# Kernel optimization log

Hardware: AMD Instinct MI355X
Metric: run time of the kernel (lower is better)

Reference implementation:

```python
import math
import jax, jax.numpy as jnp
import numpy as np

N = 50000          # nodes
E = 1_600_000      # edges
DNE = 128
DED = 128
NUM_RBF = 50
R_CUT = 5.0
LN_EPS = 1e-5


def setup_inputs() -> dict:
    key = jax.random.key(0)
    ks = jax.random.split(key, 16)
    z = jax.random.normal(ks[0], (N, 25), jnp.float32)
    edge = jax.random.randint(ks[1], (E, 2), 0, N, dtype=jnp.int64)
    r = jax.random.uniform(ks[2], (E,), jnp.float32) * (R_CUT * 1.1)  # some beyond cutoff
    u_raw = jax.random.normal(ks[3], (E, 3), jnp.float32)
    u = u_raw / jnp.linalg.norm(u_raw, axis=-1, keepdims=True)

    def xavier(k, shape):
        fan_in, fan_out = shape
        lim = math.sqrt(6.0 / (fan_in + fan_out))
        return jax.random.uniform(k, shape, jnp.float32, -lim, lim)

    return {
        "z": z, "edge": edge, "r": r, "u": u,
        "A_na_w": xavier(ks[4], (25, DNE)), "A_na_b": jnp.zeros((DNE,), jnp.float32),
        "A_nbr_w": xavier(ks[5], (25, DNE)), "A_nbr_b": jnp.zeros((DNE,), jnp.float32),
        "W_ndp_w": xavier(ks[6], (NUM_RBF, DNE)), "W_ndp_b": jnp.zeros((DNE,), jnp.float32),
        "W_nrd_w": xavier(ks[7], (2 * DNE, DNE)), "W_nrd_b": jnp.zeros((DNE,), jnp.float32),
        "W_nru_w": xavier(ks[8], (DNE, DNE)), "W_nru_b": jnp.zeros((DNE,), jnp.float32),
        "W_erp_w": xavier(ks[9], (NUM_RBF, DED)), "W_erp_b": jnp.zeros((DED,), jnp.float32),
        "ln_g": jnp.ones((DNE,), jnp.float32), "ln_b": jnp.zeros((DNE,), jnp.float32),
    }


def _sh_l2(u):
    x, y, zc = u[:, 0], u[:, 1], u[:, 2]
    s3 = math.sqrt(3.0)
    return jnp.stack([
        s3 * x * y,
        s3 * y * zc,
        0.5 * (3.0 * zc * zc - 1.0),
        s3 * zc * x,
        0.5 * s3 * (x * x - y * y),
    ], axis=-1)  # [E, 5]


def _rbf(r):
    start = math.exp(-R_CUT)
    means = jnp.linspace(start, 1.0, NUM_RBF)
    beta = (2.0 / NUM_RBF * (1.0 - start)) ** (-2)
    alpha = 5.0 / R_CUT
    return jnp.exp(-beta * (jnp.exp(-alpha * r[:, None]) - means) ** 2)  # [E, NUM_RBF]


def reference(z, edge, r, u,
              A_na_w, A_na_b, A_nbr_w, A_nbr_b,
              W_ndp_w, W_ndp_b, W_nrd_w, W_nrd_b,
              W_nru_w, W_nru_b, W_erp_w, W_erp_b,
              ln_g, ln_b):
    i, j = edge[:, 0], edge[:, 1]
    n_nodes = z.shape[0]

    # edge tensor representations (Lmax=2)
    rt0 = r[:, None]          # [E,1]
    rt1 = u                   # [E,3]
    rt2 = _sh_l2(u)           # [E,5]

    rbf = _rbf(r)                                              # [E,R]
    c = (0.5 * (jnp.cos(math.pi * r / R_CUT) + 1.0)
         * (r < R_CUT).astype(r.dtype))[:, None]               # [E,1]

    nbr = jax.nn.silu(z @ A_nbr_w + A_nbr_b)                   # [N,dne]
    gate = (rbf @ W_ndp_w + W_ndp_b) * c                       # [E,dne]
    msg = nbr[j] * gate                                        # gather + gate
    m = jax.ops.segment_sum(msg, i, num_segments=n_nodes)      # scatter-add [N,dne]

    na = jax.nn.silu(z @ A_na_w + A_na_b)
    h = jnp.concatenate([na, m], axis=-1) @ W_nrd_w + W_nrd_b  # [N,dne]
    mu = jnp.mean(h, axis=-1, keepdims=True)
    var = jnp.var(h, axis=-1, keepdims=True)
    h = (h - mu) / jnp.sqrt(var + LN_EPS) * ln_g + ln_b
    h = jax.nn.silu(h)
    h = h @ W_nru_w + W_nru_b                                  # [N,dne]

    t = (h[i] + h[j]) * (rbf @ W_erp_w + W_erp_b)              # [E,ded]
    return (h, t, rt0, rt1, rt2, c)
```

## Files before the change

### kernel.cpp

```cpp
#include <hip/hip_runtime.h>
#include <hip/hip_bf16.h>
#include <math.h>

#define NN 50000
#define NE 1600000
#define D 128
#define NRBF 50
#define RCUT 5.0f
#define LNEPS 1e-5f
#define SCAN_B 196
#define NB 16
#define NPW 8
#define EO_GRID 2048

typedef __attribute__((ext_vector_type(8))) short bf16x8;
typedef __attribute__((ext_vector_type(4))) float f32x4;

__device__ __forceinline__ float silu_f(float x) {
    return x / (1.0f + __expf(-x));
}
__device__ __forceinline__ unsigned short f2bf(float x) {
    __hip_bfloat16 b = __float2bfloat16(x);
    return *reinterpret_cast<unsigned short*>(&b);
}
__device__ __forceinline__ float bf2f(unsigned short u) {
    unsigned int x = ((unsigned int)u) << 16;
    return __uint_as_float(x);
}

__global__ __launch_bounds__(128) void nbr_kernel(
    const float* __restrict__ z, const float* __restrict__ Aw,
    const float* __restrict__ Ab, unsigned short* __restrict__ nbr_bf)
{
    const int n = blockIdx.x;
    const int d = threadIdx.x;
    float acc = Ab[d];
#pragma unroll
    for (int k = 0; k < 25; ++k)
        acc = fmaf(z[n * 25 + k], Aw[k * D + d], acc);
    nbr_bf[(size_t)n * D + d] = f2bf(silu_f(acc));
}

__global__ __launch_bounds__(256) void aux_kernel(
    const int* __restrict__ edge, const float* __restrict__ r,
    const float* __restrict__ u, float* __restrict__ rt0,
    float* __restrict__ rt1, float* __restrict__ rt2,
    float* __restrict__ cout, int* __restrict__ cnt)
{
    const int e = blockIdx.x * 256 + threadIdx.x;
    if (e >= NE) return;
    const float rr = r[e];
    __builtin_nontemporal_store(rr, &rt0[e]);
    const float cc = (rr < RCUT)
        ? 0.5f * (__cosf(3.14159265358979f * rr * (1.0f / RCUT)) + 1.0f)
        : 0.0f;
    __builtin_nontemporal_store(cc, &cout[e]);
    const float x  = u[e * 3 + 0];
    const float y  = u[e * 3 + 1];
    const float zc = u[e * 3 + 2];
    __builtin_nontemporal_store(x,  &rt1[(size_t)e * 3 + 0]);
    __builtin_nontemporal_store(y,  &rt1[(size_t)e * 3 + 1]);
    __builtin_nontemporal_store(zc, &rt1[(size_t)e * 3 + 2]);
    const float s3 = 1.7320508075688772f;
    __builtin_nontemporal_store(s3 * x * y,                  &rt2[(size_t)e * 5 + 0]);
    __builtin_nontemporal_store(s3 * y * zc,                 &rt2[(size_t)e * 5 + 1]);
    __builtin_nontemporal_store(0.5f * (3.0f * zc * zc - 1.0f), &rt2[(size_t)e * 5 + 2]);
    __builtin_nontemporal_store(s3 * zc * x,                 &rt2[(size_t)e * 5 + 3]);
    __builtin_nontemporal_store(0.5f * s3 * (x * x - y * y), &rt2[(size_t)e * 5 + 4]);
    atomicAdd(&cnt[edge[2 * e]], 1);
}

__global__ __launch_bounds__(256) void scan1_kernel(
    const int* __restrict__ cnt, int* __restrict__ off, int* __restrict__ bsum)
{
    __shared__ int s[2][256];
    const int t = threadIdx.x;
    const int g = blockIdx.x * 256 + t;
    const int v = (g < NN) ? cnt[g] : 0;
    int incl = v;
    s[0][t] = incl;
    __syncthreads();
    int cur = 0;
#pragma unroll
    for (int dd = 1; dd < 256; dd <<= 1) {
        const int add = (t >= dd) ? s[cur][t - dd] : 0;
        incl += add;
        s[cur ^ 1][t] = incl;
        __syncthreads();
        cur ^= 1;
    }
    if (g < NN) off[g] = incl - v;
    if (t == 255) bsum[blockIdx.x] = incl;
}

__global__ __launch_bounds__(256) void scan2_kernel(int* __restrict__ bsum)
{
    __shared__ int s[2][256];
    const int t = threadIdx.x;
    const int v = (t < SCAN_B) ? bsum[t] : 0;
    int incl = v;
    s[0][t] = incl;
    __syncthreads();
    int cur = 0;
#pragma unroll
    for (int dd = 1; dd < 256; dd <<= 1) {
        const int add = (t >= dd) ? s[cur][t - dd] : 0;
        incl += add;
        s[cur ^ 1][t] = incl;
        __syncthreads();
        cur ^= 1;
    }
    if (t < SCAN_B) bsum[t] = incl - v;
}

__global__ __launch_bounds__(256) void scan3_kernel(
    int* __restrict__ off, const int* __restrict__ bsum)
{
    const int g = blockIdx.x * 256 + threadIdx.x;
    if (g < NN) off[g] += bsum[blockIdx.x];
    if (g == 0) off[NN] = NE;
}

__global__ __launch_bounds__(256) void scatter_kernel(
    const int* __restrict__ edge, const float* __restrict__ r,
    const int* __restrict__ off, int* __restrict__ cursor,
    uint2* __restrict__ jr)
{
    const int e = blockIdx.x * 256 + threadIdx.x;
    if (e >= NE) return;
    const int2 ep = ((const int2*)edge)[e];
    const int pos = atomicAdd(&cursor[ep.x], 1);
    uint2 v;
    v.x = (unsigned int)ep.y;
    v.y = __float_as_uint(r[e]);
    jr[off[ep.x] + pos] = v;
}

__global__ __launch_bounds__(256) void gather_msg_wave(
    const uint2* __restrict__ jr, const int* __restrict__ off,
    const float* __restrict__ W_ndp, const float* __restrict__ b_ndp,
    const unsigned short* __restrict__ nbr_bf, float* __restrict__ m)
{
    const int tid = threadIdx.x;
    const int w   = tid >> 6;
    const int l   = tid & 63;
    const int lr  = l & 15;
    const int lg  = l >> 4;

    bf16x8 wf[8][2];
#pragma unroll
    for (int dt = 0; dt < 8; ++dt) {
        const int col = lr * 8 + dt;
#pragma unroll
        for (int s = 0; s < 2; ++s) {
            bf16x8 v;
#pragma unroll
            for (int j = 0; j < 8; ++j) {
                const int k = s * 32 + lg * 8 + j;
                float wv = 0.0f;
                if (k < NRBF)       wv = W_ndp[k * D + col];
                else if (k == NRBF) wv = b_ndp[col];
                v[j] = (short)f2bf(wv);
            }
            wf[dt][s] = v;
        }
    }

    const float start = expf(-RCUT);
    const float step  = (1.0f - start) / (NRBF - 1);
    const float bq    = (2.0f / NRBF) * (1.0f - start);
    const float beta  = 1.0f / (bq * bq);

    const int wid = blockIdx.x * 4 + w;

    for (int nn = 0; nn < NPW; ++nn) {
        const int n = wid * NPW + nn;
        if (n >= NN) break;
        const int s0  = off[n];
        const int deg = off[n + 1] - s0;

        f32x4 macc[8] = {{0,0,0,0},{0,0,0,0},{0,0,0,0},{0,0,0,0},
                         {0,0,0,0},{0,0,0,0},{0,0,0,0},{0,0,0,0}};

        for (int base = 0; base < deg; base += 16) {
            unsigned int jv = 0;
            float er = 0.0f, cc = 0.0f;
            if (l < 16 && l < deg - base) {
                const uint2 v = jr[s0 + base + l];
                jv = v.x;
                const float rr = __uint_as_float(v.y);
                er = __expf(-rr);
                cc = (rr < RCUT)
                    ? 0.5f * (__cosf(3.14159265358979f * rr * (1.0f / RCUT)) + 1.0f)
                    : 0.0f;
            }
            const float erL = __shfl(er, lr);
            const float ccL = __shfl(cc, lr);

            bf16x8 af[2];
#pragma unroll
            for (int s = 0; s < 2; ++s) {
                bf16x8 a;
#pragma unroll
                for (int j = 0; j < 8; ++j) {
                    const int k = s * 32 + lg * 8 + j;
                    float pv = 0.0f;
                    if (k < NRBF) {
                        const float diff = erL - (start + (float)k * step);
                        pv = ccL * __expf(-beta * diff * diff);
                    } else if (k == NRBF) {
                        pv = ccL;
                    }
                    a[j] = (short)f2bf(pv);
                }
                af[s] = a;
            }

            f32x4 accs[8];
#pragma unroll
            for (int dt = 0; dt < 8; ++dt) {
                f32x4 acc = {0.0f, 0.0f, 0.0f, 0.0f};
                acc = __builtin_amdgcn_mfma_f32_16x16x32_bf16(af[0], wf[dt][0], acc, 0, 0, 0);
                acc = __builtin_amdgcn_mfma_f32_16x16x32_bf16(af[1], wf[dt][1], acc, 0, 0, 0);
                accs[dt] = acc;
            }
#pragma unroll
            for (int q = 0; q < 4; ++q) {
                const int jrow = __shfl((int)jv, lg * 4 + q);
                const bf16x8 nv8 = *(const bf16x8*)(nbr_bf + (size_t)jrow * D + lr * 8);
#pragma unroll
                for (int dt = 0; dt < 8; ++dt)
                    macc[dt][q] = fmaf(bf2f((unsigned short)nv8[dt]), accs[dt][q], macc[dt][q]);
            }
        }

        float vv[8];
#pragma unroll
        for (int dt = 0; dt < 8; ++dt) {
            float v = macc[dt][0] + macc[dt][1] + macc[dt][2] + macc[dt][3];
            v += __shfl_xor(v, 16);
            v += __shfl_xor(v, 32);
            vv[dt] = v;
        }
        if (lg == 0) {
            f32x4 o0 = {vv[0], vv[1], vv[2], vv[3]};
            f32x4 o1 = {vv[4], vv[5], vv[6], vv[7]};
            float* mp = &m[(size_t)n * D + lr * 8];
            *(f32x4*)mp       = o0;
            *(f32x4*)(mp + 4) = o1;
        }
    }
}

__global__ __launch_bounds__(256) void node_kernel2(
    const float* __restrict__ z, const float* __restrict__ A_na_w,
    const float* __restrict__ A_na_b, const float* __restrict__ m,
    const float* __restrict__ W_nrd_w, const float* __restrict__ W_nrd_b,
    const float* __restrict__ W_nru_w, const float* __restrict__ W_nru_b,
    const float* __restrict__ ln_g, const float* __restrict__ ln_b,
    float* __restrict__ hout, unsigned short* __restrict__ h_bf)
{
    __shared__ float inbuf[NB][260];
    __shared__ float wbuf[32][128];
    __shared__ float part[4][NB][2];

    const int tid = threadIdx.x;
    const int n0 = blockIdx.x * NB;
    const int nl = tid & 15;
    const int dg = tid >> 4;

    for (int idx = tid; idx < NB * 128; idx += 256) {
        const int n = idx >> 7;
        const int d = idx & 127;
        float acc = A_na_b[d];
#pragma unroll
        for (int k = 0; k < 25; ++k)
            acc = fmaf(z[(size_t)(n0 + n) * 25 + k], A_na_w[k * D + d], acc);
        inbuf[n][d]       = silu_f(acc);
        inbuf[n][128 + d] = m[(size_t)(n0 + n) * D + d];
    }

    float h1[8];
#pragma unroll
    for (int dd = 0; dd < 8; ++dd) h1[dd] = W_nrd_b[dg * 8 + dd];

    for (int tile = 0; tile < 8; ++tile) {
        __syncthreads();
        for (int v = tid; v < 32 * 32; v += 256) {
            const int row = v >> 5;
            const int c4  = (v & 31) * 4;
            *(float4*)&wbuf[row][c4] =
                *(const float4*)&W_nrd_w[(size_t)(tile * 32 + row) * D + c4];
        }
        __syncthreads();
#pragma unroll 4
        for (int k = 0; k < 32; ++k) {
            const float rin = inbuf[nl][tile * 32 + k];
            const float4 wa = *(const float4*)&wbuf[k][dg * 8];
            const float4 wb = *(const float4*)&wbuf[k][dg * 8 + 4];
            h1[0] = fmaf(rin, wa.x, h1[0]);
            h1[1] = fmaf(rin, wa.y, h1[1]);
            h1[2] = fmaf(rin, wa.z, h1[2]);
            h1[3] = fmaf(rin, wa.w, h1[3]);
            h1[4] = fmaf(rin, wb.x, h1[4]);
            h1[5] = fmaf(rin, wb.y, h1[5]);
            h1[6] = fmaf(rin, wb.z, h1[6]);
            h1[7] = fmaf(rin, wb.w, h1[7]);
        }
    }

    float s = 0.0f, sq = 0.0f;
#pragma unroll
    for (int dd = 0; dd < 8; ++dd) { s += h1[dd]; sq += h1[dd] * h1[dd]; }
    s  += __shfl_xor(s, 16);  sq += __shfl_xor(sq, 16);
    s  += __shfl_xor(s, 32);  sq += __shfl_xor(sq, 32);
    const int wv = tid >> 6;
    if ((tid & 63) < 16) { part[wv][nl][0] = s; part[wv][nl][1] = sq; }
    __syncthreads();
    float ts = 0.0f, tsq = 0.0f;
#pragma unroll
    for (int w = 0; w < 4; ++w) { ts += part[w][nl][0]; tsq += part[w][nl][1]; }
    const float mu  = ts * (1.0f / 128.0f);
    const float var = tsq * (1.0f / 128.0f) - mu * mu;
    const float inv = rsqrtf(var + LNEPS);

#pragma unroll
    for (int dd = 0; dd < 8; ++dd) {
        const int d = dg * 8 + dd;
        inbuf[nl][d] = silu_f((h1[dd] - mu) * inv * ln_g[d] + ln_b[d]);
    }

    float h2[8];
#pragma unroll
    for (int dd = 0; dd < 8; ++dd) h2[dd] = W_nru_b[dg * 8 + dd];

    for (int tile = 0; tile < 4; ++tile) {
        __syncthreads();
        for (int v = tid; v < 32 * 32; v += 256) {
            const int row = v >> 5;
            const int c4  = (v & 31) * 4;
            *(float4*)&wbuf[row][c4] =
                *(const float4*)&W_nru_w[(size_t)(tile * 32 + row) * D + c4];
        }
        __syncthreads();
#pragma unroll 4
        for (int k = 0; k < 32; ++k) {
            const float rin = inbuf[nl][tile * 32 + k];
            const float4 wa = *(const float4*)&wbuf[k][dg * 8];
            const float4 wb = *(const float4*)&wbuf[k][dg * 8 + 4];
            h2[0] = fmaf(rin, wa.x, h2[0]);
            h2[1] = fmaf(rin, wa.y, h2[1]);
            h2[2] = fmaf(rin, wa.z, h2[2]);
            h2[3] = fmaf(rin, wa.w, h2[3]);
            h2[4] = fmaf(rin, wb.x, h2[4]);
            h2[5] = fmaf(rin, wb.y, h2[5]);
            h2[6] = fmaf(rin, wb.z, h2[6]);
            h2[7] = fmaf(rin, wb.w, h2[7]);
        }
    }

    f32x4 o0 = {h2[0], h2[1], h2[2], h2[3]};
    f32x4 o1 = {h2[4], h2[5], h2[6], h2[7]};
    float* hp = &hout[(size_t)(n0 + nl) * D + dg * 8];
    __builtin_nontemporal_store(o0, (f32x4*)hp);
    __builtin_nontemporal_store(o1, (f32x4*)(hp + 4));

    unsigned int b0 = (unsigned int)f2bf(h2[0]) | ((unsigned int)f2bf(h2[1]) << 16);
    unsigned int b1 = (unsigned int)f2bf(h2[2]) | ((unsigned int)f2bf(h2[3]) << 16);
    unsigned int b2 = (unsigned int)f2bf(h2[4]) | ((unsigned int)f2bf(h2[5]) << 16);
    unsigned int b3 = (unsigned int)f2bf(h2[6]) | ((unsigned int)f2bf(h2[7]) << 16);
    *(uint4*)&h_bf[(size_t)(n0 + nl) * D + dg * 8] = make_uint4(b0, b1, b2, b3);
}

__global__ __launch_bounds__(256) void edge_out_wave(
    const int* __restrict__ edge, const float* __restrict__ r,
    const float* __restrict__ W_erp, const float* __restrict__ b_erp,
    const unsigned short* __restrict__ h_bf, float* __restrict__ t)
{
    const int tid = threadIdx.x;
    const int w   = tid >> 6;
    const int l   = tid & 63;
    const int lr  = l & 15;
    const int lg  = l >> 4;

    bf16x8 wf[8][2];
    float bias[8];
#pragma unroll
    for (int dt = 0; dt < 8; ++dt) {
        const int col = lr * 8 + dt;
        bias[dt] = b_erp[col];
#pragma unroll
        for (int s = 0; s < 2; ++s) {
            bf16x8 v;
#pragma unroll
            for (int j = 0; j < 8; ++j) {
                const int k = s * 32 + lg * 8 + j;
                v[j] = (k < NRBF) ? (short)f2bf(W_erp[k * D + col]) : (short)0;
            }
            wf[dt][s] = v;
        }
    }

    const float start = expf(-RCUT);
    const float step  = (1.0f - start) / (NRBF - 1);
    const float bq    = (2.0f / NRBF) * (1.0f - start);
    const float beta  = 1.0f / (bq * bq);

    const int wid = blockIdx.x * 4 + w;
    const int nw  = gridDim.x * 4;
    const int ngroup = NE / 16;

    for (int g = wid; g < ngroup; g += nw) {
        const int eb = g * 16;
        int iv = 0, jv = 0;
        float er = 0.0f;
        if (l < 16) {
            const int2 ep = ((const int2*)edge)[eb + l];
            iv = ep.x;
            jv = ep.y;
            er = __expf(-r[eb + l]);
        }
        const float erL = __shfl(er, lr);

        bf16x8 af[2];
#pragma unroll
        for (int s = 0; s < 2; ++s) {
            bf16x8 a;
#pragma unroll
            for (int j = 0; j < 8; ++j) {
                const int k = s * 32 + lg * 8 + j;
                float pv = 0.0f;
                if (k < NRBF) {
                    const float diff = erL - (start + (float)k * step);
                    pv = __expf(-beta * diff * diff);
                }
                a[j] = (short)f2bf(pv);
            }
            af[s] = a;
        }

        f32x4 accs[8];
#pragma unroll
        for (int dt = 0; dt < 8; ++dt) {
            f32x4 acc = {0.0f, 0.0f, 0.0f, 0.0f};
            acc = __builtin_amdgcn_mfma_f32_16x16x32_bf16(af[0], wf[dt][0], acc, 0, 0, 0);
            acc = __builtin_amdgcn_mfma_f32_16x16x32_bf16(af[1], wf[dt][1], acc, 0, 0, 0);
            accs[dt] = acc;
        }

#pragma unroll
        for (int q = 0; q < 4; ++q) {
            const int irow = __shfl(iv, lg * 4 + q);
            const int jrow = __shfl(jv, lg * 4 + q);
            const bf16x8 hi8 = *(const bf16x8*)(h_bf + (size_t)irow * D + lr * 8);
            const bf16x8 hj8 = *(const bf16x8*)(h_bf + (size_t)jrow * D + lr * 8);
            float o[8];
#pragma unroll
            for (int dt = 0; dt < 8; ++dt) {
                const float hvf = bf2f((unsigned short)hi8[dt]) + bf2f((unsigned short)hj8[dt]);
                o[dt] = hvf * (accs[dt][q] + bias[dt]);
            }
            f32x4 o0 = {o[0], o[1], o[2], o[3]};
            f32x4 o1 = {o[4], o[5], o[6], o[7]};
            float* tp = &t[(size_t)(eb + lg * 4 + q) * D + lr * 8];
            __builtin_nontemporal_store(o0, (f32x4*)tp);
            __builtin_nontemporal_store(o1, (f32x4*)(tp + 4));
        }
    }
}

extern "C" void kernel_launch(void* const* d_in, const int* in_sizes, int n_in,
                              void* d_out, int out_size, void* d_ws, size_t ws_size,
                              hipStream_t stream) {
    const float* z      = (const float*)d_in[0];
    const int*   edge   = (const int*)d_in[1];
    const float* r      = (const float*)d_in[2];
    const float* u      = (const float*)d_in[3];
    const float* A_na_w  = (const float*)d_in[4];
    const float* A_na_b  = (const float*)d_in[5];
    const float* A_nbr_w = (const float*)d_in[6];
    const float* A_nbr_b = (const float*)d_in[7];
    const float* W_ndp_w = (const float*)d_in[8];
    const float* W_ndp_b = (const float*)d_in[9];
    const float* W_nrd_w = (const float*)d_in[10];
    const float* W_nrd_b = (const float*)d_in[11];
    const float* W_nru_w = (const float*)d_in[12];
    const float* W_nru_b = (const float*)d_in[13];
    const float* W_erp_w = (const float*)d_in[14];
    const float* W_erp_b = (const float*)d_in[15];
    const float* ln_g    = (const float*)d_in[16];
    const float* ln_b    = (const float*)d_in[17];

    float* out = (float*)d_out;
    float* h_out   = out;
    float* t_out   = out + (size_t)NN * D;
    float* rt0_out = t_out + (size_t)NE * D;
    float* rt1_out = rt0_out + (size_t)NE;
    float* rt2_out = rt1_out + (size_t)NE * 3;
    float* c_out   = rt2_out + (size_t)NE * 5;

    unsigned short* nbr_bf = (unsigned short*)d_ws;
    float* m_ws   = (float*)((char*)d_ws + (size_t)NN * D * sizeof(unsigned short));
    unsigned short* h_bf = (unsigned short*)((char*)m_ws + (size_t)NN * D * sizeof(float));

    uint2* jr   = (uint2*)t_out;
    int* off    = (int*)(jr + NE);
    int* cursor = off + (NN + 1);
    int* bsum   = cursor + NN;

    hipMemsetAsync(cursor, 0, (size_t)NN * sizeof(int), stream);

    nbr_kernel<<<NN, 128, 0, stream>>>(z, A_nbr_w, A_nbr_b, nbr_bf);

    aux_kernel<<<(NE + 255) / 256, 256, 0, stream>>>(
        edge, r, u, rt0_out, rt1_out, rt2_out, c_out, cursor);

    scan1_kernel<<<SCAN_B, 256, 0, stream>>>(cursor, off, bsum);
    scan2_kernel<<<1, 256, 0, stream>>>(bsum);
    scan3_kernel<<<SCAN_B, 256, 0, stream>>>(off, bsum);

    hipMemsetAsync(cursor, 0, (size_t)NN * sizeof(int), stream);

    scatter_kernel<<<(NE + 255) / 256, 256, 0, stream>>>(edge, r, off, cursor, jr);

    {
        const int nwaves = (NN + NPW - 1) / NPW;
        const int blocks = (nwaves + 3) / 4;
        gather_msg_wave<<<blocks, 256, 0, stream>>>(
            jr, off, W_ndp_w, W_ndp_b, nbr_bf, m_ws);
    }

    node_kernel2<<<NN / NB, 256, 0, stream>>>(
        z, A_na_w, A_na_b, m_ws, W_nrd_w, W_nrd_b,
        W_nru_w, W_nru_b, ln_g, ln_b, h_out, h_bf);

    edge_out_wave<<<EO_GRID, 256, 0, stream>>>(
        edge, r, W_erp_w, W_erp_b, h_bf, t_out);
}
```

Measured before the change: 832.2 us.

## Prefetch next edge indices and issue row gathers before MFMA in gather and edge kernels

In both the message-gather and edge-output kernels, the next iteration's edge indices and radii are loaded one step ahead (software prefetch). The neighbour-row gathers are issued before the RBF and MFMA computation so their latency overlaps with that math. Launch bounds now request at least 3 blocks per CU, which caps register use. The extra live registers for prefetched values, combined with the tighter register cap, could cause spilling.

```diff
diff --git a/kernel.cpp b/kernel.cpp
--- a/kernel.cpp
+++ b/kernel.cpp
@@ -136,7 +136,7 @@
     jr[off[ep.x] + pos] = v;
 }
 
-__global__ __launch_bounds__(256) void gather_msg_wave(
+__global__ __launch_bounds__(256, 3) void gather_msg_wave(
     const uint2* __restrict__ jr, const int* __restrict__ off,
     const float* __restrict__ W_ndp, const float* __restrict__ b_ndp,
     const unsigned short* __restrict__ nbr_bf, float* __restrict__ m)
@@ -182,20 +182,37 @@
         f32x4 macc[8] = {{0,0,0,0},{0,0,0,0},{0,0,0,0},{0,0,0,0},
                          {0,0,0,0},{0,0,0,0},{0,0,0,0},{0,0,0,0}};
 
+        uint2 v = make_uint2(0u, 0u);
+        if (l < 16 && l < deg) v = jr[s0 + l];
+
         for (int base = 0; base < deg; base += 16) {
-            unsigned int jv = 0;
+            const bool val = (l < 16) && (base + l < deg);
+            const unsigned int jv = val ? v.x : 0u;
             float er = 0.0f, cc = 0.0f;
-            if (l < 16 && l < deg - base) {
-                const uint2 v = jr[s0 + base + l];
-                jv = v.x;
+            if (val) {
                 const float rr = __uint_as_float(v.y);
                 er = __expf(-rr);
                 cc = (rr < RCUT)
                     ? 0.5f * (__cosf(3.14159265358979f * rr * (1.0f / RCUT)) + 1.0f)
                     : 0.0f;
             }
+            uint2 vn = make_uint2(0u, 0u);
+            if (l < 16 && base + 16 + l < deg) vn = jr[s0 + base + 16 + l];
+
             const float erL = __shfl(er, lr);
             const float ccL = __shfl(cc, lr);
+
+            bf16x8 nv0, nv1, nv2, nv3;
+            {
+                const int j0 = __shfl((int)jv, lg * 4 + 0);
+                const int j1 = __shfl((int)jv, lg * 4 + 1);
+                const int j2 = __shfl((int)jv, lg * 4 + 2);
+                const int j3 = __shfl((int)jv, lg * 4 + 3);
+                nv0 = *(const bf16x8*)(nbr_bf + (size_t)j0 * D + lr * 8);
+                nv1 = *(const bf16x8*)(nbr_bf + (size_t)j1 * D + lr * 8);
+                nv2 = *(const bf16x8*)(nbr_bf + (size_t)j2 * D + lr * 8);
+                nv3 = *(const bf16x8*)(nbr_bf + (size_t)j3 * D + lr * 8);
+            }
 
             bf16x8 af[2];
 #pragma unroll
@@ -216,31 +233,26 @@
                 af[s] = a;
             }
 
-            f32x4 accs[8];
 #pragma unroll
             for (int dt = 0; dt < 8; ++dt) {
                 f32x4 acc = {0.0f, 0.0f, 0.0f, 0.0f};
                 acc = __builtin_amdgcn_mfma_f32_16x16x32_bf16(af[0], wf[dt][0], acc, 0, 0, 0);
                 acc = __builtin_amdgcn_mfma_f32_16x16x32_bf16(af[1], wf[dt][1], acc, 0, 0, 0);
-                accs[dt] = acc;
-            }
-#pragma unroll
-            for (int q = 0; q < 4; ++q) {
-                const int jrow = __shfl((int)jv, lg * 4 + q);
-                const bf16x8 nv8 = *(const bf16x8*)(nbr_bf + (size_t)jrow * D + lr * 8);
-#pragma unroll
-                for (int dt = 0; dt < 8; ++dt)
-                    macc[dt][q] = fmaf(bf2f((unsigned short)nv8[dt]), accs[dt][q], macc[dt][q]);
-            }
+                macc[dt][0] = fmaf(bf2f((unsigned short)nv0[dt]), acc[0], macc[dt][0]);
+                macc[dt][1] = fmaf(bf2f((unsigned short)nv1[dt]), acc[1], macc[dt][1]);
+                macc[dt][2] = fmaf(bf2f((unsigned short)nv2[dt]), acc[2], macc[dt][2]);
+                macc[dt][3] = fmaf(bf2f((unsigned short)nv3[dt]), acc[3], macc[dt][3]);
+            }
+            v = vn;
         }
 
         float vv[8];
 #pragma unroll
         for (int dt = 0; dt < 8; ++dt) {
-            float v = macc[dt][0] + macc[dt][1] + macc[dt][2] + macc[dt][3];
-            v += __shfl_xor(v, 16);
-            v += __shfl_xor(v, 32);
-            vv[dt] = v;
+            float x = macc[dt][0] + macc[dt][1] + macc[dt][2] + macc[dt][3];
+            x += __shfl_xor(x, 16);
+            x += __shfl_xor(x, 32);
+            vv[dt] = x;
         }
         if (lg == 0) {
             f32x4 o0 = {vv[0], vv[1], vv[2], vv[3]};
@@ -372,7 +384,7 @@
     *(uint4*)&h_bf[(size_t)(n0 + nl) * D + dg * 8] = make_uint4(b0, b1, b2, b3);
 }
 
-__global__ __launch_bounds__(256) void edge_out_wave(
+__global__ __launch_bounds__(256, 3) void edge_out_wave(
     const int* __restrict__ edge, const float* __restrict__ r,
     const float* __restrict__ W_erp, const float* __restrict__ b_erp,
     const unsigned short* __restrict__ h_bf, float* __restrict__ t)
@@ -410,17 +422,42 @@
     const int nw  = gridDim.x * 4;
     const int ngroup = NE / 16;
 
+    int2 ep = make_int2(0, 0);
+    float rv = 0.0f;
+    if (wid < ngroup && l < 16) {
+        ep = ((const int2*)edge)[wid * 16 + l];
+        rv = r[wid * 16 + l];
+    }
+
     for (int g = wid; g < ngroup; g += nw) {
-        const int eb = g * 16;
-        int iv = 0, jv = 0;
-        float er = 0.0f;
-        if (l < 16) {
-            const int2 ep = ((const int2*)edge)[eb + l];
-            iv = ep.x;
-            jv = ep.y;
-            er = __expf(-r[eb + l]);
-        }
+        const int iv = ep.x;
+        const int jv = ep.y;
+        const float er = __expf(-rv);
+
+        int2 epn = make_int2(0, 0);
+        float rvn = 0.0f;
+        if (g + nw < ngroup && l < 16) {
+            epn = ((const int2*)edge)[(g + nw) * 16 + l];
+            rvn = r[(g + nw) * 16 + l];
+        }
+
         const float erL = __shfl(er, lr);
+
+        bf16x8 hi0, hi1, hi2, hi3, hj0, hj1, hj2, hj3;
+        {
+            const int i0 = __shfl(iv, lg * 4 + 0), j0 = __shfl(jv, lg * 4 + 0);
+            const int i1 = __shfl(iv, lg * 4 + 1), j1 = __shfl(jv, lg * 4 + 1);
+            const int i2 = __shfl(iv, lg * 4 + 2), j2 = __shfl(jv, lg * 4 + 2);
+            const int i3 = __shfl(iv, lg * 4 + 3), j3 = __shfl(jv, lg * 4 + 3);
+            hi0 = *(const bf16x8*)(h_bf + (size_t)i0 * D + lr * 8);
+            hj0 = *(const bf16x8*)(h_bf + (size_t)j0 * D + lr * 8);
+            hi1 = *(const bf16x8*)(h_bf + (size_t)i1 * D + lr * 8);
+            hj1 = *(const bf16x8*)(h_bf + (size_t)j1 * D + lr * 8);
+            hi2 = *(const bf16x8*)(h_bf + (size_t)i2 * D + lr * 8);
+            hj2 = *(const bf16x8*)(h_bf + (size_t)j2 * D + lr * 8);
+            hi3 = *(const bf16x8*)(h_bf + (size_t)i3 * D + lr * 8);
+            hj3 = *(const bf16x8*)(h_bf + (size_t)j3 * D + lr * 8);
+        }
 
         bf16x8 af[2];
 #pragma unroll
@@ -448,12 +485,11 @@
             accs[dt] = acc;
         }
 
+        const int eb = g * 16;
 #pragma unroll
         for (int q = 0; q < 4; ++q) {
-            const int irow = __shfl(iv, lg * 4 + q);
-            const int jrow = __shfl(jv, lg * 4 + q);
-            const bf16x8 hi8 = *(const bf16x8*)(h_bf + (size_t)irow * D + lr * 8);
-            const bf16x8 hj8 = *(const bf16x8*)(h_bf + (size_t)jrow * D + lr * 8);
+            const bf16x8 hi8 = (q == 0) ? hi0 : (q == 1) ? hi1 : (q == 2) ? hi2 : hi3;
+            const bf16x8 hj8 = (q == 0) ? hj0 : (q == 1) ? hj1 : (q == 2) ? hj2 : hj3;
             float o[8];
 #pragma unroll
             for (int dt = 0; dt < 8; ++dt) {
@@ -466,6 +502,9 @@
             __builtin_nontemporal_store(o0, (f32x4*)tp);
             __builtin_nontemporal_store(o1, (f32x4*)(tp + 4));
         }
+
+        ep = epn;
+        rv = rvn;
     }
 }
 
```

Measured after the change: 840.5 us (median of 2 runs). About the same (+1.0%).
